# Kernel tuning notes

Hardware: AMD Instinct MI355X
Metric: run time of the kernel (lower is better)

The kernel has to match this reference:

```python
import jax, jax.numpy as jnp
import numpy as np

N, E, F, H, C = 100000, 1600000, 128, 16, 8


def _gcn_conv(x, src, dst, ew, W, b, n):
    """PyG GCNConv with edge_weight: x@W, add self-loops (weight 1),
    symmetric degree normalization, scatter-add to destination, + bias."""
    h = x @ W                                   # [n, out]
    loop = jnp.arange(n)
    s = jnp.concatenate([src, loop])
    d = jnp.concatenate([dst, loop])
    w = jnp.concatenate([ew, jnp.ones((n,), ew.dtype)])
    deg = jax.ops.segment_sum(w, d, num_segments=n)          # in-degree by edge weight
    dis = jnp.where(deg > 0, jax.lax.rsqrt(deg), 0.0)        # deg^-1/2, inf -> 0
    norm = dis[s] * w * dis[d]                               # [E+n]
    out = jax.ops.segment_sum(h[s] * norm[:, None], d, num_segments=n)
    return out + b


def setup_inputs() -> dict:
    key = jax.random.key(0)
    ks = jax.random.split(key, 7)
    x = jax.random.normal(ks[0], (N, F), dtype=jnp.float32)
    edge_index = jax.random.randint(ks[1], (2, E), 0, N, dtype=jnp.int64)
    edge_attr = jax.random.uniform(ks[2], (E,), dtype=jnp.float32)
    W1 = jax.random.normal(ks[3], (F, H), dtype=jnp.float32) * (1.0 / np.sqrt(F))
    b1 = jnp.zeros((H,), jnp.float32)
    W2 = jax.random.normal(ks[4], (H, C), dtype=jnp.float32) * (1.0 / np.sqrt(H))
    b2 = jnpps = jnp.zeros((C,), jnp.float32)
    return {"x": x, "edge_index": edge_index, "edge_attr": edge_attr,
            "W1": W1, "b1": b1, "W2": W2, "b2": b2}


def reference(x, edge_index, edge_attr, W1, b1, W2, b2):
    n = x.shape[0]
    src, dst = edge_index[0], edge_index[1]
    h = jax.nn.relu(_gcn_conv(x, src, dst, edge_attr, W1, b1, n))
    # F.dropout(training=self.training): identity in eval mode (deterministic ref)
    return _gcn_conv(h, src, dst, edge_attr, W2, b2, n)
```

## Files before the change

kernel.cpp:

```cpp
#include <hip/hip_runtime.h>

#define F_IN  128
#define H_MID 16
#define C_OUT 8
#define XS_PAD (F_IN + 4)
#define TROWS 32
#define CHUNK 4096
#define NBMAX 512
#define CAP   8192
#define GEMM_SHF (2 * TROWS * XS_PAD + F_IN * H_MID)

__global__ void __launch_bounds__(512) k_zero512(int* __restrict__ p) {
    p[threadIdx.x] = 0;
}

__device__ __forceinline__ void gemm1_part(
        const float* __restrict__ x, const float* __restrict__ W1,
        float* __restrict__ h1, int N, int t0, int t1, int j, int S,
        float* __restrict__ arena) {
    float* xs  = arena;
    float* W1s = arena + 2 * TROWS * XS_PAD;
    const int t = threadIdx.x;
    for (int i = t; i < F_IN * H_MID; i += 256) W1s[i] = W1[i];
    const int c  = t & 15;
    const int r0 = t >> 4;
    int tile = t0 + j;
    if (tile >= t1) return;

    float4 st[4];
    auto stage_load = [&](int tl) {
        const float4* xg = reinterpret_cast<const float4*>(x + (long long)tl * TROWS * F_IN);
        const int nfl = ((N - tl * TROWS < TROWS) ? (N - tl * TROWS) : TROWS) * (F_IN / 4);
#pragma unroll
        for (int k = 0; k < 4; ++k) {
            const int i = t + k * 256;
            st[k] = (i < nfl) ? xg[i] : make_float4(0.f, 0.f, 0.f, 0.f);
        }
    };
    auto stage_write = [&](int buf) {
#pragma unroll
        for (int k = 0; k < 4; ++k) {
            const int i = t + k * 256;
            *reinterpret_cast<float4*>(&xs[buf * TROWS * XS_PAD + (i >> 5) * XS_PAD + (i & 31) * 4]) = st[k];
        }
    };

    stage_load(tile);
    stage_write(0);
    __syncthreads();
    int buf = 0;
    while (true) {
        const int next = tile + S;
        if (next < t1) stage_load(next);
        const float* xr0 = &xs[buf * TROWS * XS_PAD + r0 * XS_PAD];
        const float* xr1 = xr0 + 16 * XS_PAD;
        float acc0 = 0.0f, acc1 = 0.0f;
#pragma unroll 4
        for (int k4 = 0; k4 < F_IN / 4; ++k4) {
            const float4 v0 = *reinterpret_cast<const float4*>(&xr0[k4 * 4]);
            const float4 v1 = *reinterpret_cast<const float4*>(&xr1[k4 * 4]);
            const float w0 = W1s[(k4 * 4 + 0) * H_MID + c];
            const float w1 = W1s[(k4 * 4 + 1) * H_MID + c];
            const float w2 = W1s[(k4 * 4 + 2) * H_MID + c];
            const float w3 = W1s[(k4 * 4 + 3) * H_MID + c];
            acc0 = fmaf(v0.x, w0, acc0); acc1 = fmaf(v1.x, w0, acc1);
            acc0 = fmaf(v0.y, w1, acc0); acc1 = fmaf(v1.y, w1, acc1);
            acc0 = fmaf(v0.z, w2, acc0); acc1 = fmaf(v1.z, w2, acc1);
            acc0 = fmaf(v0.w, w3, acc0); acc1 = fmaf(v1.w, w3, acc1);
        }
        const long long row0 = (long long)tile * TROWS + r0;
        const long long row1 = row0 + 16;
        if (row0 < N) h1[row0 * H_MID + c] = acc0;
        if (row1 < N) h1[row1 * H_MID + c] = acc1;
        if (next >= t1) break;
        __syncthreads();
        stage_write(buf ^ 1);
        __syncthreads();
        buf ^= 1;
        tile = next;
    }
}

__global__ void __launch_bounds__(256) k_build_g(
        const int* __restrict__ src, const int* __restrict__ dst,
        const float* __restrict__ ew, int* __restrict__ bcursor,
        int2* __restrict__ bed, int E, int NB,
        const float* __restrict__ x, const float* __restrict__ W1,
        float* __restrict__ h1, int N, int t0, int t1, int NCSR, int NG) {
    struct S {
        int hist4[4][NBMAX];
        int cur4[4][NBMAX];
        int scn[NBMAX], tot[NBMAX], base[NBMAX];
        int2 sorted[CHUNK];
        unsigned short bof[CHUNK];
    };
    union Shm { S s; float g[GEMM_SHF]; };
    __shared__ Shm u;
    const int b = blockIdx.x;
    if (b >= NCSR) { gemm1_part(x, W1, h1, N, t0, t1, b - NCSR, NG, u.g); return; }

    const int t = threadIdx.x;
    const int w = t >> 6;
    const int c0 = b * CHUNK;
    const int n = (E - c0 < CHUNK) ? (E - c0) : CHUNK;

    for (int l = t; l < NBMAX; l += 256) {
        u.s.hist4[0][l] = 0; u.s.hist4[1][l] = 0; u.s.hist4[2][l] = 0; u.s.hist4[3][l] = 0;
    }
    __syncthreads();
    for (int i = t; i < n; i += 256)
        atomicAdd(&u.s.hist4[w][((unsigned)dst[c0 + i]) >> 8], 1);
    __syncthreads();
    {
        const int l0 = t, l1 = t + 256;
        const int q0 = u.s.hist4[0][l0] + u.s.hist4[1][l0] + u.s.hist4[2][l0] + u.s.hist4[3][l0];
        const int q1 = u.s.hist4[0][l1] + u.s.hist4[1][l1] + u.s.hist4[2][l1] + u.s.hist4[3][l1];
        u.s.tot[l0] = q0; u.s.tot[l1] = q1;
        u.s.scn[l0] = q0; u.s.scn[l1] = q1;
    }
    __syncthreads();
#pragma unroll
    for (int off = 1; off < 512; off <<= 1) {
        const int i1 = t + 256;
        const int v0 = (t >= off) ? u.s.scn[t - off] : 0;
        const int v1 = u.s.scn[i1 - off];
        __syncthreads();
        u.s.scn[t] += v0;
        u.s.scn[i1] += v1;
        __syncthreads();
    }
    for (int l = t; l < NBMAX; l += 256) {
        int e = u.s.scn[l] - u.s.tot[l];
        u.s.cur4[0][l] = e;
        e += u.s.hist4[0][l]; u.s.cur4[1][l] = e;
        e += u.s.hist4[1][l]; u.s.cur4[2][l] = e;
        e += u.s.hist4[2][l]; u.s.cur4[3][l] = e;
    }
    __syncthreads();
    for (int i = t; i < n; i += 256) {
        const int s  = src[c0 + i];
        const int d  = dst[c0 + i];
        const float wt = ew[c0 + i];
        const int bk = ((unsigned)d) >> 8;
        const int slot = atomicAdd(&u.s.cur4[w][bk], 1);
        u.s.sorted[slot] = make_int2(s | ((d & 255) << 18), __float_as_int(wt));
        u.s.bof[slot] = (unsigned short)bk;
    }
    __syncthreads();
    for (int l = t; l < NB; l += 256)
        u.s.base[l] = u.s.tot[l] ? (l * CAP + atomicAdd(&bcursor[l], u.s.tot[l])) : 0;
    __syncthreads();
    for (int i = t; i < n; i += 256) {
        const int bk = u.s.bof[i];
        const int excl = u.s.scn[bk] - u.s.tot[bk];
        const int pos = u.s.base[bk] + (i - excl);
        if (pos < (bk + 1) * CAP) bed[pos] = u.s.sorted[i];
    }
}

__global__ void __launch_bounds__(256) k_bsort_g(
        const int2* __restrict__ bed, const int* __restrict__ bcursor,
        int2* __restrict__ rowseg, float* __restrict__ dis,
        int2* __restrict__ ed, int N, int NB,
        const float* __restrict__ x, const float* __restrict__ W1,
        float* __restrict__ h1, int t0, int t1, int NCSR, int NG) {
    struct S { int hist[256], scn[256], cur[256]; float degw[256]; };
    union Shm { S s; float g[GEMM_SHF]; };
    __shared__ Shm u;
    const int b = blockIdx.x;
    if (b >= NCSR) { gemm1_part(x, W1, h1, N, t0, t1, b - NCSR, NG, u.g); return; }

    const int t = threadIdx.x;
    const int r0 = b << 8;
    const int L = (N - r0 < 256) ? (N - r0) : 256;
    const int e0 = b * CAP;
    int M = bcursor[b];
    if (M > CAP) M = CAP;

    u.s.hist[t] = 0;
    u.s.degw[t] = 0.0f;
    __syncthreads();
    for (int i = t; i < M; i += 256) {
        const int2 rec = bed[e0 + i];
        const int dl = ((unsigned)rec.x) >> 18;
        atomicAdd(&u.s.hist[dl], 1);
        atomicAdd(&u.s.degw[dl], __int_as_float(rec.y));
    }
    __syncthreads();
    u.s.scn[t] = u.s.hist[t];
    __syncthreads();
#pragma unroll
    for (int off = 1; off < 256; off <<= 1) {
        int v = (t >= off) ? u.s.scn[t - off] : 0;
        __syncthreads();
        u.s.scn[t] += v;
        __syncthreads();
    }
    const int excl = u.s.scn[t] - u.s.hist[t];
    if (t < L) {
        rowseg[r0 + t] = make_int2(e0 + excl, e0 + u.s.scn[t]);
        dis[r0 + t] = rsqrtf(1.0f + u.s.degw[t]);
    }
    u.s.cur[t] = excl;
    __syncthreads();
    for (int i = t; i < M; i += 256) {
        const int2 rec = bed[e0 + i];
        const int dl = ((unsigned)rec.x) >> 18;
        const int slot = atomicAdd(&u.s.cur[dl], 1);
        ed[e0 + slot] = make_int2(rec.x & 0x3FFFF, rec.y);
    }
}


__global__ void __launch_bounds__(256) k_agg16f(
        const int2* __restrict__ rowseg, const int2* __restrict__ ed,
        const float* __restrict__ h, const float* __restrict__ dis,
        const float* __restrict__ b1, const float* __restrict__ W2,
        float* __restrict__ h2s, int N) {
    __shared__ float W2s[H_MID * C_OUT];
    if (threadIdx.x < H_MID * C_OUT) W2s[threadIdx.x] = W2[threadIdx.x];
    __syncthreads();
    const long long tg = (long long)blockIdx.x * 256 + threadIdx.x;
    const int node = (int)(tg >> 4);
    const int c = (int)(tg & 15);
    if (node >= N) return;
    const int2 seg = rowseg[node];
    const float dn = dis[node];
    float a0 = h[(long long)node * H_MID + c] * dn;
    float a1 = 0.f, a2 = 0.f, a3 = 0.f;
    int e = seg.x;
    for (; e + 3 < seg.y; e += 4) {
        const int2 p0 = ed[e],     p1 = ed[e + 1];
        const int2 p2 = ed[e + 2], p3 = ed[e + 3];
        const float w0 = __int_as_float(p0.y) * dis[p0.x];
        const float w1 = __int_as_float(p1.y) * dis[p1.x];
        const float w2 = __int_as_float(p2.y) * dis[p2.x];
        const float w3 = __int_as_float(p3.y) * dis[p3.x];
        a0 = fmaf(h[(long long)p0.x * H_MID + c], w0, a0);
        a1 = fmaf(h[(long long)p1.x * H_MID + c], w1, a1);
        a2 = fmaf(h[(long long)p2.x * H_MID + c], w2, a2);
        a3 = fmaf(h[(long long)p3.x * H_MID + c], w3, a3);
    }
    for (; e < seg.y; ++e) {
        const int2 p = ed[e];
        a0 = fmaf(h[(long long)p.x * H_MID + c], __int_as_float(p.y) * dis[p.x], a0);
    }
    float r = fmaf((a0 + a1) + (a2 + a3), dn, b1[c]);
    r = fmaxf(r, 0.0f);
    float h2 = 0.0f;
#pragma unroll
    for (int cc = 0; cc < H_MID; ++cc) {
        const float rc = __shfl(r, cc, 16);
        h2 = fmaf(rc, W2s[cc * C_OUT + (c & 7)], h2);
    }
    if (c < C_OUT) h2s[(long long)node * C_OUT + c] = h2 * dn;
}

__global__ void __launch_bounds__(256) k_agg8(
        const int2* __restrict__ rowseg, const int2* __restrict__ ed,
        const float* __restrict__ h, const float* __restrict__ dis,
        const float* __restrict__ b2, float* __restrict__ out, int N) {
    const long long tg = (long long)blockIdx.x * 256 + threadIdx.x;
    const int node = (int)(tg >> 3);
    const int c = (int)(tg & 7);
    if (node >= N) return;
    const int2 seg = rowseg[node];
    float a0 = h[(long long)node * C_OUT + c];
    float a1 = 0.f, a2 = 0.f, a3 = 0.f;
    int e = seg.x;
    for (; e + 3 < seg.y; e += 4) {
        const int2 p0 = ed[e],     p1 = ed[e + 1];
        const int2 p2 = ed[e + 2], p3 = ed[e + 3];
        a0 = fmaf(h[(long long)p0.x * C_OUT + c], __int_as_float(p0.y), a0);
        a1 = fmaf(h[(long long)p1.x * C_OUT + c], __int_as_float(p1.y), a1);
        a2 = fmaf(h[(long long)p2.x * C_OUT + c], __int_as_float(p2.y), a2);
        a3 = fmaf(h[(long long)p3.x * C_OUT + c], __int_as_float(p3.y), a3);
    }
    for (; e < seg.y; ++e) {
        const int2 p = ed[e];
        a0 = fmaf(h[(long long)p.x * C_OUT + c], __int_as_float(p.y), a0);
    }
    out[(long long)node * C_OUT + c] = fmaf((a0 + a1) + (a2 + a3), dis[node], b2[c]);
}

__global__ void k_init_deg(float* __restrict__ deg, int N) {
    int i = blockIdx.x * blockDim.x + threadIdx.x;
    if (i < N) deg[i] = 1.0f;
}
__global__ void k_scatter_deg(const int* __restrict__ dst, const float* __restrict__ ew,
                              float* __restrict__ deg, int E) {
    int e = blockIdx.x * blockDim.x + threadIdx.x;
    if (e < E) atomicAdd(&deg[dst[e]], ew[e]);
}
__global__ void k_rsqrt(float* __restrict__ deg, int N) {
    int i = blockIdx.x * blockDim.x + threadIdx.x;
    if (i < N) {
        float v = deg[i];
        deg[i] = (v > 0.0f) ? rsqrtf(v) : 0.0f;
    }
}
__global__ void k_gemm1_r2(const float* __restrict__ x, const float* __restrict__ W1,
                           const float* __restrict__ b1, const float* __restrict__ dis,
                           float* __restrict__ h1, float* __restrict__ a1, int N) {
    __shared__ float W1s[F_IN * H_MID];
    for (int i = threadIdx.x; i < F_IN * H_MID; i += blockDim.x) W1s[i] = W1[i];
    __syncthreads();
    const int c   = threadIdx.x & 15;
    const int lr  = threadIdx.x >> 4;
    const int rpb = blockDim.x >> 4;
    for (long long row = (long long)blockIdx.x * rpb + lr; row < N;
         row += (long long)gridDim.x * rpb) {
        const float4* xr = reinterpret_cast<const float4*>(x + row * F_IN);
        float acc = 0.0f;
#pragma unroll
        for (int k4 = 0; k4 < F_IN / 4; ++k4) {
            float4 v = xr[k4];
            acc = fmaf(v.x, W1s[(k4 * 4 + 0) * H_MID + c], acc);
            acc = fmaf(v.y, W1s[(k4 * 4 + 1) * H_MID + c], acc);
            acc = fmaf(v.z, W1s[(k4 * 4 + 2) * H_MID + c], acc);
            acc = fmaf(v.w, W1s[(k4 * 4 + 3) * H_MID + c], acc);
        }
        h1[row * H_MID + c] = acc;
        float di = dis[row];
        a1[row * H_MID + c] = fmaf(acc, di * di, b1[c]);
    }
}
template <int CH>
__global__ void k_agg_at(const int* __restrict__ src, const int* __restrict__ dst,
                         const float* __restrict__ ew, const float* __restrict__ dis,
                         const float* __restrict__ h, float* __restrict__ out, long long E) {
    const int LOG = (CH == 16) ? 4 : 3;
    const long long total  = E << LOG;
    const long long stride = (long long)gridDim.x * blockDim.x;
    for (long long idx = (long long)blockIdx.x * blockDim.x + threadIdx.x; idx < total;
         idx += stride) {
        const long long e = idx >> LOG;
        const int c = (int)(idx & (CH - 1));
        const int s = src[e];
        const int d = dst[e];
        const float norm = dis[s] * ew[e] * dis[d];
        atomicAdd(out + (long long)d * CH + c, h[(long long)s * CH + c] * norm);
    }
}
__global__ void k_gemm2_r2(const float* __restrict__ a1, const float* __restrict__ W2,
                           const float* __restrict__ b2, const float* __restrict__ dis,
                           float* __restrict__ h2, float* __restrict__ out, int N) {
    __shared__ float W2s[H_MID * C_OUT];
    if (threadIdx.x < H_MID * C_OUT) W2s[threadIdx.x] = W2[threadIdx.x];
    __syncthreads();
    const int c   = threadIdx.x & 7;
    const int lr  = threadIdx.x >> 3;
    const int rpb = blockDim.x >> 3;
    for (long long row = (long long)blockIdx.x * rpb + lr; row < N;
         row += (long long)gridDim.x * rpb) {
        const float4* ar = reinterpret_cast<const float4*>(a1 + row * H_MID);
        float acc = 0.0f;
#pragma unroll
        for (int k4 = 0; k4 < H_MID / 4; ++k4) {
            float4 v = ar[k4];
            acc = fmaf(fmaxf(v.x, 0.0f), W2s[(k4 * 4 + 0) * C_OUT + c], acc);
            acc = fmaf(fmaxf(v.y, 0.0f), W2s[(k4 * 4 + 1) * C_OUT + c], acc);
            acc = fmaf(fmaxf(v.z, 0.0f), W2s[(k4 * 4 + 2) * C_OUT + c], acc);
            acc = fmaf(fmaxf(v.w, 0.0f), W2s[(k4 * 4 + 3) * C_OUT + c], acc);
        }
        h2[row * C_OUT + c] = acc;
        float di = dis[row];
        out[row * C_OUT + c] = fmaf(acc, di * di, b2[c]);
    }
}

extern "C" void kernel_launch(void* const* d_in, const int* in_sizes, int n_in,
                              void* d_out, int out_size, void* d_ws, size_t ws_size,
                              hipStream_t stream) {
    const float* x  = (const float*)d_in[0];
    const int*   ei = (const int*)d_in[1];
    const float* ew = (const float*)d_in[2];
    const float* W1 = (const float*)d_in[3];
    const float* b1 = (const float*)d_in[4];
    const float* W2 = (const float*)d_in[5];
    const float* b2 = (const float*)d_in[6];
    float* out = (float*)d_out;

    const int H   = in_sizes[4];
    const int Fin = in_sizes[3] / H;
    const int N   = in_sizes[0] / Fin;
    const int E   = in_sizes[2];
    const int* src = ei;
    const int* dst = ei + E;
    (void)n_in; (void)out_size;

    char* ws = (char*)d_ws;
    size_t off = 0;
    auto alloc = [&](size_t bytes) {
        void* p = ws + off;
        off = (off + bytes + 255) & ~(size_t)255;
        return p;
    };
    float* dis    = (float*)alloc((size_t)N * sizeof(float));
    float* h1     = (float*)alloc((size_t)N * H_MID * sizeof(float));
    int2*  rowseg = (int2*)alloc((size_t)N * sizeof(int2));
    int*   bcursor= (int*)alloc(NBMAX * sizeof(int));
    const int NB  = (N + 255) >> 8;
    int2*  bed    = (int2*)alloc((size_t)NB * CAP * sizeof(int2));
    int2*  ed     = (int2*)alloc((size_t)NB * CAP * sizeof(int2));
    float* h2s = (float*)bed;
    const size_t needed = off;

    const int B = 256;
    const int NCH = (E + CHUNK - 1) / CHUNK;
    const bool fast_ok = (needed <= ws_size) && (N <= 131072) && (NB <= NBMAX) &&
                         (2 * ((E + NB - 1) / NB) <= CAP) &&
                         ((size_t)NB * CAP * sizeof(int2) >= (size_t)N * C_OUT * sizeof(float));

    if (fast_ok) {
        const int ntiles = (N + TROWS - 1) / TROWS;
        const int tA = (int)((long long)ntiles * 65 / 100);
        const int GB_S = 200, GB_B = 150;

        k_zero512<<<1, 512, 0, stream>>>(bcursor);
        k_build_g<<<NCH + GB_S, B, 0, stream>>>(src, dst, ew, bcursor, bed, E, NB,
                                                x, W1, h1, N, 0, tA, NCH, GB_S);
        k_bsort_g<<<NB + GB_B, B, 0, stream>>>(bed, bcursor, rowseg, dis, ed, N, NB,
                                               x, W1, h1, tA, ntiles, NB, GB_B);
        k_agg16f<<<(int)(((long long)N * H_MID + B - 1) / B), B, 0, stream>>>(
            rowseg, ed, h1, dis, b1, W2, h2s, N);
        k_agg8<<<(int)(((long long)N * C_OUT + B - 1) / B), B, 0, stream>>>(
            rowseg, ed, h2s, dis, b2, out, N);
    } else {
        off = 0;
        float* disF = (float*)alloc((size_t)N * sizeof(float));
        float* h1F  = (float*)alloc((size_t)N * H_MID * sizeof(float));
        float* a1F  = (float*)alloc((size_t)N * H_MID * sizeof(float));
        float* h2   = (float*)alloc((size_t)N * C_OUT * sizeof(float));
        k_init_deg<<<(N + B - 1) / B, B, 0, stream>>>(disF, N);
        k_scatter_deg<<<(E + B - 1) / B, B, 0, stream>>>(dst, ew, disF, E);
        k_rsqrt<<<(N + B - 1) / B, B, 0, stream>>>(disF, N);
        k_gemm1_r2<<<(N + 15) / 16, B, 0, stream>>>(x, W1, b1, disF, h1F, a1F, N);
        k_agg_at<H_MID><<<8192, B, 0, stream>>>(src, dst, ew, disF, h1F, a1F, E);
        k_gemm2_r2<<<(N + 31) / 32, B, 0, stream>>>(a1F, W2, b2, disF, h2, out, N);
        k_agg_at<C_OUT><<<8192, B, 0, stream>>>(src, dst, ew, disF, h2, out, E);
    }
}
```

Baseline: 136.6 us.

## Use single shared histogram in bucket build and rebalance GEMM block counts

Replaces the per-wavefront (4-way) shared-memory histograms and cursors in the edge bucketing kernel with a single histogram and cursor array, removing the merge step and shrinking shared memory. This lowers the LDS footprint and setup work but raises atomic contention on shared counters. It also sizes the co-scheduled GEMM block counts so each fused launch totals about 768 blocks, and moves the tile split between the two launches from 65% to 60%.

```diff
diff --git a/kernel.cpp b/kernel.cpp
--- a/kernel.cpp
+++ b/kernel.cpp
@@ -88,9 +88,7 @@
         const float* __restrict__ x, const float* __restrict__ W1,
         float* __restrict__ h1, int N, int t0, int t1, int NCSR, int NG) {
     struct S {
-        int hist4[4][NBMAX];
-        int cur4[4][NBMAX];
-        int scn[NBMAX], tot[NBMAX], base[NBMAX];
+        int hist[NBMAX], scn[NBMAX], cur[NBMAX], base[NBMAX];
         int2 sorted[CHUNK];
         unsigned short bof[CHUNK];
     };
@@ -100,24 +98,16 @@
     if (b >= NCSR) { gemm1_part(x, W1, h1, N, t0, t1, b - NCSR, NG, u.g); return; }
 
     const int t = threadIdx.x;
-    const int w = t >> 6;
     const int c0 = b * CHUNK;
     const int n = (E - c0 < CHUNK) ? (E - c0) : CHUNK;
 
-    for (int l = t; l < NBMAX; l += 256) {
-        u.s.hist4[0][l] = 0; u.s.hist4[1][l] = 0; u.s.hist4[2][l] = 0; u.s.hist4[3][l] = 0;
-    }
+    for (int l = t; l < NBMAX; l += 256) u.s.hist[l] = 0;
     __syncthreads();
     for (int i = t; i < n; i += 256)
-        atomicAdd(&u.s.hist4[w][((unsigned)dst[c0 + i]) >> 8], 1);
-    __syncthreads();
-    {
-        const int l0 = t, l1 = t + 256;
-        const int q0 = u.s.hist4[0][l0] + u.s.hist4[1][l0] + u.s.hist4[2][l0] + u.s.hist4[3][l0];
-        const int q1 = u.s.hist4[0][l1] + u.s.hist4[1][l1] + u.s.hist4[2][l1] + u.s.hist4[3][l1];
-        u.s.tot[l0] = q0; u.s.tot[l1] = q1;
-        u.s.scn[l0] = q0; u.s.scn[l1] = q1;
-    }
+        atomicAdd(&u.s.hist[((unsigned)dst[c0 + i]) >> 8], 1);
+    __syncthreads();
+    u.s.scn[t] = u.s.hist[t];
+    u.s.scn[t + 256] = u.s.hist[t + 256];
     __syncthreads();
 #pragma unroll
     for (int off = 1; off < 512; off <<= 1) {
@@ -129,30 +119,25 @@
         u.s.scn[i1] += v1;
         __syncthreads();
     }
-    for (int l = t; l < NBMAX; l += 256) {
-        int e = u.s.scn[l] - u.s.tot[l];
-        u.s.cur4[0][l] = e;
-        e += u.s.hist4[0][l]; u.s.cur4[1][l] = e;
-        e += u.s.hist4[1][l]; u.s.cur4[2][l] = e;
-        e += u.s.hist4[2][l]; u.s.cur4[3][l] = e;
-    }
+    u.s.cur[t] = u.s.scn[t] - u.s.hist[t];
+    u.s.cur[t + 256] = u.s.scn[t + 256] - u.s.hist[t + 256];
     __syncthreads();
     for (int i = t; i < n; i += 256) {
         const int s  = src[c0 + i];
         const int d  = dst[c0 + i];
         const float wt = ew[c0 + i];
         const int bk = ((unsigned)d) >> 8;
-        const int slot = atomicAdd(&u.s.cur4[w][bk], 1);
+        const int slot = atomicAdd(&u.s.cur[bk], 1);
         u.s.sorted[slot] = make_int2(s | ((d & 255) << 18), __float_as_int(wt));
         u.s.bof[slot] = (unsigned short)bk;
     }
     __syncthreads();
     for (int l = t; l < NB; l += 256)
-        u.s.base[l] = u.s.tot[l] ? (l * CAP + atomicAdd(&bcursor[l], u.s.tot[l])) : 0;
+        u.s.base[l] = u.s.hist[l] ? (l * CAP + atomicAdd(&bcursor[l], u.s.hist[l])) : 0;
     __syncthreads();
     for (int i = t; i < n; i += 256) {
         const int bk = u.s.bof[i];
-        const int excl = u.s.scn[bk] - u.s.tot[bk];
+        const int excl = u.s.scn[bk] - u.s.hist[bk];
         const int pos = u.s.base[bk] + (i - excl);
         if (pos < (bk + 1) * CAP) bed[pos] = u.s.sorted[i];
     }
@@ -414,8 +399,9 @@
 
     if (fast_ok) {
         const int ntiles = (N + TROWS - 1) / TROWS;
-        const int tA = (int)((long long)ntiles * 65 / 100);
-        const int GB_S = 200, GB_B = 150;
+        const int GB_S = (NCH < 704) ? (768 - NCH) : 64;
+        const int GB_B = (NB  < 704) ? (768 - NB)  : 64;
+        const int tA = (int)((long long)ntiles * 60 / 100);
 
         k_zero512<<<1, 512, 0, stream>>>(bcursor);
         k_build_g<<<NCH + GB_S, B, 0, stream>>>(src, dst, ew, bcursor, bed, E, NB,
```

Measured after the change: 111.5 us, median of 2. 18.4% less time.
